# Optimization experiments

Hardware: AMD Instinct MI355X
Metric: run time of the kernel (lower is better)

## Reference

```python
import jax, jax.numpy as jnp
import numpy as np

B, N, D, K = 16, 1024, 512, 16  # batch graphs, nodes/graph, feat dim, knn k
NEG_SLOPE = 0.2


def setup_inputs() -> dict:
    key = jax.random.key(0)
    ks = jax.random.split(key, 16)
    s = 1.0 / np.sqrt(D)
    p = {}
    p["x"] = jax.random.normal(ks[0], (B, N, D), dtype=jnp.float32)
    for i, l in enumerate(["1", "2", "3"]):
        p["W" + l] = jax.random.normal(ks[1 + 4 * i], (D, D), dtype=jnp.float32) * s
        p["asrc" + l] = jax.random.normal(ks[2 + 4 * i], (D,), dtype=jnp.float32) * s
        p["adst" + l] = jax.random.normal(ks[3 + 4 * i], (D,), dtype=jnp.float32) * s
        p["b" + l] = jnp.zeros((D,), dtype=jnp.float32)
    p["Wc"] = jax.random.normal(ks[13], (D, 2), dtype=jnp.float32) * s
    p["bc"] = jnp.zeros((2,), dtype=jnp.float32)
    return p


def _knn_idx(pos):
    # pos: [N, D]. k nearest neighbors by euclidean distance, self excluded
    sq = jnp.sum(pos * pos, axis=1)
    d2 = sq[:, None] + sq[None, :] - 2.0 * (pos @ pos.T)  # [N, N]
    d2 = jnp.where(jnp.eye(N, dtype=bool), jnp.inf, d2)
    _, idx = jax.lax.top_k(-d2, K)  # [N, K] neighbor (source) indices per node
    return idx


def _normalize_scale(pos):
    # PyG NormalizeScale: center, then scale so max abs coord ~ 1
    pos = pos - pos.mean(axis=0, keepdims=True)
    return pos * (0.999999 / jnp.max(jnp.abs(pos)))


def _gat(h, nbr, W, asrc, adst, b):
    # GATConv, 1 head, self-loops already included in nbr [N, K+1]
    hp = h @ W                                   # [N, D]
    a_s = hp @ asrc                              # [N] att for sources
    a_d = hp @ adst                              # [N] att for targets
    e = jax.nn.leaky_relu(a_s[nbr] + a_d[:, None], NEG_SLOPE)  # [N, K+1]
    att = jax.nn.softmax(e, axis=-1)             # softmax over each node's in-edges
    msg = hp[nbr]                                # [N, K+1, D] gathered neighbor feats
    return jnp.einsum('nk,nkd->nd', att, msg) + b


def reference(x, W1, asrc1, adst1, b1, W2, asrc2, adst2, b2, W3, asrc3, adst3, b3, Wc, bc):
    self_idx = jnp.arange(N)[:, None]

    def per_graph(pos):
        nbr = jnp.concatenate([_knn_idx(pos), self_idx], axis=1)  # [N, K+1] w/ self-loop
        h = _normalize_scale(pos)
        h = jax.nn.relu(_gat(h, nbr, W1, asrc1, adst1, b1))
        h = jax.nn.relu(_gat(h, nbr, W2, asrc2, adst2, b2))
        h = _gat(h, nbr, W3, asrc3, adst3, b3)
        return h.max(axis=0)  # global max pool over nodes

    g = jax.vmap(per_graph)(x)  # [B, D]
    return g @ Wc + bc          # [B, 2]
```

## Files before the change

kernel.cpp:

```cpp
#include <hip/hip_runtime.h>
#include <hip/hip_bf16.h>
#include <math.h>

#define BATCH 16
#define NNODE 1024
#define DIM   512
#define KNN   16
#define KP1   17
#define NCAND 18
#define NEG   0.2f
#define BT    128
#define NCH   16

typedef __attribute__((ext_vector_type(8))) short bf16x8;
typedef __attribute__((ext_vector_type(4))) float f32x4;

#define GLOAD16(g, l) __builtin_amdgcn_global_load_lds( \
    (const __attribute__((address_space(1))) unsigned int*)(g), \
    (__attribute__((address_space(3))) unsigned int*)(l), 16, 0, 0)

__device__ __forceinline__ unsigned short f2bf(float f) {
    unsigned u = __float_as_uint(f);
    unsigned r = (u + 0x7FFFu + ((u >> 16) & 1u)) >> 16;
    return (unsigned short)r;
}
__device__ __forceinline__ float bf2f(unsigned short h) {
    return __uint_as_float(((unsigned)h) << 16);
}
__device__ __forceinline__ void split_store(float v, unsigned short* hi, unsigned short* lo, size_t idx) {
    unsigned short h = f2bf(v);
    hi[idx] = h;
    lo[idx] = f2bf(v - bf2f(h));
}

__global__ void init_misc(unsigned* __restrict__ maxabs, unsigned* __restrict__ genc) {
    int gid = blockIdx.x * 256 + threadIdx.x;
    if (gid < BATCH) maxabs[gid] = 0u;
    if (gid < BATCH * DIM) genc[gid] = 0u;
}

__global__ __launch_bounds__(256) void colmean_part(const float* __restrict__ x, float* __restrict__ part) {
    int b = blockIdx.x, dc = blockIdx.y, ch = blockIdx.z;
    int d = dc * 256 + threadIdx.x;
    const float* p = x + ((size_t)b * NNODE + ch * (NNODE / NCH)) * DIM + d;
    float s = 0.f;
    #pragma unroll 4
    for (int n = 0; n < NNODE / NCH; ++n) s += p[(size_t)n * DIM];
    part[((size_t)b * NCH + ch) * DIM + d] = s;
}
__global__ void colmean_fin(const float* __restrict__ part, float* __restrict__ mean) {
    int id = blockIdx.x * 256 + threadIdx.x;
    int b = id >> 9, d = id & (DIM - 1);
    float s = 0.f;
    #pragma unroll
    for (int ch = 0; ch < NCH; ++ch) s += part[((size_t)b * NCH + ch) * DIM + d];
    mean[id] = s * (1.0f / NNODE);
}

__global__ __launch_bounds__(256) void rowsq_xtobf(const float* __restrict__ x,
                                                   float* __restrict__ sq,
                                                   unsigned short* __restrict__ xh) {
    int row = blockIdx.x * 4 + (threadIdx.x >> 6);
    int l = threadIdx.x & 63;
    const float* p = x + (size_t)row * DIM + l * 8;
    float4 a = *(const float4*)p;
    float4 b = *(const float4*)(p + 4);
    float s = a.x * a.x + a.y * a.y + a.z * a.z + a.w * a.w
            + b.x * b.x + b.y * b.y + b.z * b.z + b.w * b.w;
    ushort4 ha, hb;
    ha.x = f2bf(a.x); ha.y = f2bf(a.y); ha.z = f2bf(a.z); ha.w = f2bf(a.w);
    hb.x = f2bf(b.x); hb.y = f2bf(b.y); hb.z = f2bf(b.z); hb.w = f2bf(b.w);
    unsigned short* q = xh + (size_t)row * DIM + l * 8;
    *(ushort4*)q = ha;
    *(ushort4*)(q + 4) = hb;
    #pragma unroll
    for (int off = 32; off > 0; off >>= 1) s += __shfl_down(s, off, 64);
    if (l == 0) sq[row] = s;
}

__global__ __launch_bounds__(256, 2) void dist_mfma(const unsigned short* __restrict__ xh,
                                                    const float* __restrict__ sq,
                                                    unsigned* __restrict__ keys) {
    __shared__ unsigned short AhL[128][32], BhL[128][32];
    int mt = blockIdx.y;
    int b = mt >> 3;
    int m0 = mt * BT;
    int n0 = blockIdx.x * BT;
    int bn0 = b * NNODE + n0;
    int t = threadIdx.x;
    int lane = t & 63, w = t >> 6;
    int wm = (w >> 1) * 64, wn = (w & 1) * 64;
    int fr = lane & 15, fk = (lane >> 4) * 8;
    f32x4 acc[4][4];
    #pragma unroll
    for (int i = 0; i < 4; ++i)
        #pragma unroll
        for (int j = 0; j < 4; ++j) acc[i][j] = (f32x4){0.f, 0.f, 0.f, 0.f};

    for (int k0 = 0; k0 < DIM; k0 += 32) {
        if (k0) __syncthreads();
        #pragma unroll
        for (int p = 0; p < 2; ++p) {
            int u = t + p * 256;
            int row = u >> 2, sl = u & 3;
            int gseg = (sl ^ ((row >> 1) & 3)) * 8;
            GLOAD16(xh + (size_t)(m0 + row) * DIM + k0 + gseg, &AhL[0][0] + u * 8);
            GLOAD16(xh + (size_t)(bn0 + row) * DIM + k0 + gseg, &BhL[0][0] + u * 8);
        }
        __syncthreads();
        bf16x8 ah[4], bh[4];
        #pragma unroll
        for (int i = 0; i < 4; ++i) {
            int ra = wm + i * 16 + fr;
            int sa = (((fk >> 3) ^ ((ra >> 1) & 3)) << 3);
            ah[i] = *(const bf16x8*)&AhL[ra][sa];
            int rb = wn + i * 16 + fr;
            int sb = (((fk >> 3) ^ ((rb >> 1) & 3)) << 3);
            bh[i] = *(const bf16x8*)&BhL[rb][sb];
        }
        #pragma unroll
        for (int i = 0; i < 4; ++i)
            #pragma unroll
            for (int j = 0; j < 4; ++j)
                acc[i][j] = __builtin_amdgcn_mfma_f32_16x16x32_bf16(ah[i], bh[j], acc[i][j], 0, 0, 0);
    }
    const float* sqb = sq + b * NNODE;
    int mloc0 = m0 - b * NNODE;
    #pragma unroll
    for (int i = 0; i < 4; ++i) {
        int mloc = mloc0 + wm + i * 16 + (lane >> 4) * 4;
        #pragma unroll
        for (int j = 0; j < 4; ++j) {
            int n = n0 + wn + j * 16 + fr;
            float sqn = sqb[n];
            #pragma unroll
            for (int r = 0; r < 4; ++r) {
                float val = sqb[mloc + r] + sqn - 2.f * acc[i][j][r];
                unsigned kv = (__float_as_uint(val) & 0xFFFFFC00u) | (unsigned)n;
                if (mloc + r == n) kv = 0xFFFFFFFFu;
                keys[((size_t)b * NNODE + mloc + r) * NNODE + n] = kv;
            }
        }
    }
}

__global__ __launch_bounds__(256) void knn_kernel(const unsigned* __restrict__ keys, int* __restrict__ cand) {
    int row = blockIdx.x * 4 + (threadIdx.x >> 6);
    int l = threadIdx.x & 63;
    const unsigned* src = keys + (size_t)row * NNODE;
    unsigned key[16];
    #pragma unroll
    for (int j = 0; j < 16; ++j) key[j] = src[l + (j << 6)];
    int* dst = cand + row * NCAND;
    unsigned T = 0;
    for (int it = 0; it < NCAND; ++it) {
        unsigned lmin = 0xFFFFFFFFu;
        #pragma unroll
        for (int j = 0; j < 16; ++j) {
            unsigned k = (key[j] > T) ? key[j] : 0xFFFFFFFFu;
            lmin = min(lmin, k);
        }
        #pragma unroll
        for (int off = 1; off < 64; off <<= 1) {
            unsigned o = (unsigned)__shfl_xor((int)lmin, off, 64);
            lmin = min(lmin, o);
        }
        T = lmin;
        if (l == 0) dst[it] = (int)(lmin & 1023u);
    }
}

__global__ __launch_bounds__(256) void rerank_kernel(const float* __restrict__ x,
                                                     const float* __restrict__ sq,
                                                     const int* __restrict__ cand,
                                                     int* __restrict__ nbr) {
    int bid = blockIdx.x;
    int b = bid & (BATCH - 1);
    int w = threadIdx.x >> 6, l = threadIdx.x & 63;
    int m = (bid >> 4) * 4 + w;
    int row = b * NNODE + m;
    const float* xb = x + (size_t)b * NNODE * DIM;
    const float* sqb = sq + b * NNODE;
    const float* xm = xb + (size_t)m * DIM;
    float4 m0v = *(const float4*)(xm + l * 8);
    float4 m1v = *(const float4*)(xm + l * 8 + 4);
    float sqm = sqb[m];

    int idx[NCAND];
    #pragma unroll
    for (int c = 0; c < NCAND; ++c) idx[c] = cand[row * NCAND + c];

    float s[NCAND];
    #pragma unroll
    for (int half = 0; half < 2; ++half) {
        float4 j0[9], j1[9];
        #pragma unroll
        for (int i = 0; i < 9; ++i) {
            const float* xj = xb + (size_t)idx[half * 9 + i] * DIM;
            j0[i] = *(const float4*)(xj + l * 8);
            j1[i] = *(const float4*)(xj + l * 8 + 4);
        }
        #pragma unroll
        for (int i = 0; i < 9; ++i)
            s[half * 9 + i] = m0v.x * j0[i].x + m0v.y * j0[i].y + m0v.z * j0[i].z + m0v.w * j0[i].w
                            + m1v.x * j1[i].x + m1v.y * j1[i].y + m1v.z * j1[i].z + m1v.w * j1[i].w;
    }
    #pragma unroll
    for (int off = 32; off > 0; off >>= 1)
        #pragma unroll
        for (int c = 0; c < NCAND; ++c) s[c] += __shfl_xor(s[c], off, 64);

    unsigned long long key[NCAND];
    #pragma unroll
    for (int c = 0; c < NCAND; ++c) {
        float dv = sqm + sqb[idx[c]] - 2.f * s[c];
        key[c] = ((unsigned long long)__float_as_uint(dv) << 32) | (unsigned)idx[c];
    }
    unsigned long long mykey = ~0ull;
    int myidx = 0;
    #pragma unroll
    for (int c = 0; c < NCAND; ++c) {
        if (l == c) { mykey = key[c]; myidx = idx[c]; }
    }
    int rank = 0;
    #pragma unroll
    for (int c = 0; c < NCAND; ++c) rank += (key[c] < mykey) ? 1 : 0;

    int* dst = nbr + row * KP1;
    if (l < NCAND && rank < KNN) dst[rank] = myidx;
    if (l == 0) dst[KNN] = m;
}

__global__ __launch_bounds__(256) void maxabs_kernel(const float* __restrict__ x,
                                                     const float* __restrict__ mean,
                                                     unsigned* __restrict__ maxabs) {
    int b = blockIdx.y;
    const float* p = x + ((size_t)b * NNODE + blockIdx.x * 64) * DIM;
    const float* mb = mean + b * DIM;
    float m = 0.f;
    for (int i = threadIdx.x; i < 64 * DIM; i += 256) {
        int d = i & (DIM - 1);
        m = fmaxf(m, fabsf(p[i] - mb[d]));
    }
    __shared__ float red[256];
    red[threadIdx.x] = m; __syncthreads();
    for (int s = 128; s > 0; s >>= 1) {
        if (threadIdx.x < s) red[threadIdx.x] = fmaxf(red[threadIdx.x], red[threadIdx.x + s]);
        __syncthreads();
    }
    if (threadIdx.x == 0) atomicMax(maxabs + b, __float_as_uint(red[0]));
}

__global__ void normalize_kernel(const float* __restrict__ x, const float* __restrict__ mean,
                                 const unsigned* __restrict__ maxabs,
                                 unsigned short* __restrict__ h_hi, unsigned short* __restrict__ h_lo) {
    int id = blockIdx.x * 256 + threadIdx.x;
    int b = id >> 19;
    int d = id & (DIM - 1);
    float scale = 0.999999f / __uint_as_float(maxabs[b]);
    float v = (x[id] - mean[b * DIM + d]) * scale;
    split_store(v, h_hi, h_lo, id);
}

__global__ void wsplit_kernel(const float* __restrict__ W1, const float* __restrict__ W2,
                              const float* __restrict__ W3,
                              unsigned short* __restrict__ Wh1, unsigned short* __restrict__ Wl1,
                              unsigned short* __restrict__ Wh2, unsigned short* __restrict__ Wl2,
                              unsigned short* __restrict__ Wh3, unsigned short* __restrict__ Wl3) {
    int z = blockIdx.z;
    const float* W = (z == 0) ? W1 : (z == 1) ? W2 : W3;
    unsigned short* Wh = (z == 0) ? Wh1 : (z == 1) ? Wh2 : Wh3;
    unsigned short* Wl = (z == 0) ? Wl1 : (z == 1) ? Wl2 : Wl3;
    __shared__ float tile[32][33];
    int bx = blockIdx.x * 32, by = blockIdx.y * 32;
    int tx = threadIdx.x & 31, ty = threadIdx.x >> 5;
    #pragma unroll
    for (int i = 0; i < 4; ++i)
        tile[ty + i * 8][tx] = W[(size_t)(by + ty + i * 8) * DIM + bx + tx];
    __syncthreads();
    #pragma unroll
    for (int i = 0; i < 4; ++i) {
        int n = bx + ty + i * 8;
        float v = tile[tx][ty + i * 8];
        split_store(v, Wh, Wl, (size_t)n * DIM + by + tx);
    }
}

__global__ __launch_bounds__(256, 2) void gemm_mfma(const unsigned short* __restrict__ Agh,
                                                    const unsigned short* __restrict__ Agl,
                                                    const unsigned short* __restrict__ Bgh,
                                                    const unsigned short* __restrict__ Bgl,
                                                    const float* __restrict__ asrc,
                                                    const float* __restrict__ adst,
                                                    float* __restrict__ C,
                                                    float* __restrict__ pas,
                                                    float* __restrict__ pad) {
    __shared__ unsigned short AhL[128][32], AlL[128][32], BhL[128][32], BlL[128][32];
    __shared__ float asl[128], adl[128];
    int m0 = blockIdx.y * BT, n0 = blockIdx.x * BT;
    int t = threadIdx.x;
    int lane = t & 63, w = t >> 6;
    int wm = (w >> 1) * 64, wn = (w & 1) * 64;
    int fr = lane & 15, fk = (lane >> 4) * 8;
    f32x4 acc[4][4];
    #pragma unroll
    for (int i = 0; i < 4; ++i)
        #pragma unroll
        for (int j = 0; j < 4; ++j) acc[i][j] = (f32x4){0.f, 0.f, 0.f, 0.f};

    for (int k0 = 0; k0 < DIM; k0 += 32) {
        if (k0) __syncthreads();
        #pragma unroll
        for (int p = 0; p < 2; ++p) {
            int u = t + p * 256;
            int row = u >> 2, sl = u & 3;
            int gseg = (sl ^ ((row >> 1) & 3)) * 8;
            size_t ga = (size_t)(m0 + row) * DIM + k0 + gseg;
            size_t gb = (size_t)(n0 + row) * DIM + k0 + gseg;
            GLOAD16(Agh + ga, &AhL[0][0] + u * 8);
            GLOAD16(Agl + ga, &AlL[0][0] + u * 8);
            GLOAD16(Bgh + gb, &BhL[0][0] + u * 8);
            GLOAD16(Bgl + gb, &BlL[0][0] + u * 8);
        }
        __syncthreads();
        bf16x8 ah[4], al[4], bh[4], bl[4];
        #pragma unroll
        for (int i = 0; i < 4; ++i) {
            int ra = wm + i * 16 + fr;
            int sa = (((fk >> 3) ^ ((ra >> 1) & 3)) << 3);
            ah[i] = *(const bf16x8*)&AhL[ra][sa];
            al[i] = *(const bf16x8*)&AlL[ra][sa];
            int rb = wn + i * 16 + fr;
            int sb = (((fk >> 3) ^ ((rb >> 1) & 3)) << 3);
            bh[i] = *(const bf16x8*)&BhL[rb][sb];
            bl[i] = *(const bf16x8*)&BlL[rb][sb];
        }
        #pragma unroll
        for (int i = 0; i < 4; ++i)
            #pragma unroll
            for (int j = 0; j < 4; ++j)
                acc[i][j] = __builtin_amdgcn_mfma_f32_16x16x32_bf16(ah[i], bh[j], acc[i][j], 0, 0, 0);
        #pragma unroll
        for (int i = 0; i < 4; ++i)
            #pragma unroll
            for (int j = 0; j < 4; ++j)
                acc[i][j] = __builtin_amdgcn_mfma_f32_16x16x32_bf16(ah[i], bl[j], acc[i][j], 0, 0, 0);
        #pragma unroll
        for (int i = 0; i < 4; ++i)
            #pragma unroll
            for (int j = 0; j < 4; ++j)
                acc[i][j] = __builtin_amdgcn_mfma_f32_16x16x32_bf16(al[i], bh[j], acc[i][j], 0, 0, 0);
    }
    #pragma unroll
    for (int i = 0; i < 4; ++i) {
        int mrow = m0 + wm + i * 16 + (lane >> 4) * 4;
        #pragma unroll
        for (int j = 0; j < 4; ++j) {
            int col = n0 + wn + j * 16 + fr;
            #pragma unroll
            for (int r = 0; r < 4; ++r)
                C[(size_t)(mrow + r) * DIM + col] = acc[i][j][r];
        }
    }
    float av[4], dv[4];
    #pragma unroll
    for (int j = 0; j < 4; ++j) {
        int col = n0 + wn + j * 16 + fr;
        av[j] = asrc[col];
        dv[j] = adst[col];
    }
    if (t < 128) { asl[t] = 0.f; adl[t] = 0.f; }
    __syncthreads();
    #pragma unroll
    for (int ph = 0; ph < 2; ++ph) {
        if ((wn == 0) == (ph == 0)) {
            #pragma unroll
            for (int i = 0; i < 4; ++i)
                #pragma unroll
                for (int r = 0; r < 4; ++r) {
                    float sa = acc[i][0][r] * av[0] + acc[i][1][r] * av[1]
                             + acc[i][2][r] * av[2] + acc[i][3][r] * av[3];
                    float sd = acc[i][0][r] * dv[0] + acc[i][1][r] * dv[1]
                             + acc[i][2][r] * dv[2] + acc[i][3][r] * dv[3];
                    #pragma unroll
                    for (int off = 1; off < 16; off <<= 1) {
                        sa += __shfl_xor(sa, off, 64);
                        sd += __shfl_xor(sd, off, 64);
                    }
                    if (fr == 0) {
                        int rloc = wm + i * 16 + (lane >> 4) * 4 + r;
                        if (ph == 0) { asl[rloc] = sa;  adl[rloc] = sd; }
                        else         { asl[rloc] += sa; adl[rloc] += sd; }
                    }
                }
        }
        __syncthreads();
    }
    if (t < 128) {
        pas[(size_t)(m0 + t) * 4 + blockIdx.x] = asl[t];
        pad[(size_t)(m0 + t) * 4 + blockIdx.x] = adl[t];
    }
}

__global__ void attvec_fin(const float* __restrict__ pas, const float* __restrict__ pad,
                           float* __restrict__ as_, float* __restrict__ ad_) {
    int id = blockIdx.x * 256 + threadIdx.x;
    float4 a = *(const float4*)(pas + (size_t)id * 4);
    float4 d = *(const float4*)(pad + (size_t)id * 4);
    as_[id] = ((a.x + a.y) + a.z) + a.w;
    ad_[id] = ((d.x + d.y) + d.z) + d.w;
}

template<int RELU, int SPLIT>
__global__ __launch_bounds__(256) void aggr_kernel(const float* __restrict__ hp, const int* __restrict__ nbr,
                                                   const float* __restrict__ as_, const float* __restrict__ ad_,
                                                   const float* __restrict__ bias,
                                                   float* __restrict__ outf,
                                                   unsigned short* __restrict__ oh,
                                                   unsigned short* __restrict__ ol) {
    __shared__ float attL[4][KP1];
    __shared__ int   jjL[4][KP1];
    int bid = blockIdx.x;
    int b = bid & (BATCH - 1);
    int w = threadIdx.x >> 6, l = threadIdx.x & 63;
    int n = (bid >> 4) * 4 + w;
    int id = b * NNODE + n;

    float e = -INFINITY;
    if (l < KP1) {
        int j = nbr[id * KP1 + l];
        jjL[w][l] = j;
        e = as_[b * NNODE + j] + ad_[id];
        e = (e >= 0.f) ? e : NEG * e;
    }
    float mx = e;
    #pragma unroll
    for (int off = 16; off > 0; off >>= 1) mx = fmaxf(mx, __shfl_xor(mx, off, 64));
    float ex = (l < KP1) ? expf(e - mx) : 0.f;
    float sm = ex;
    #pragma unroll
    for (int off = 16; off > 0; off >>= 1) sm += __shfl_xor(sm, off, 64);
    if (l < KP1) attL[w][l] = ex / sm;

    const float* base = hp + (size_t)b * NNODE * DIM;
    int d0 = l * 8;
    const float4* b4 = (const float4*)(bias + d0);
    float4 o0 = b4[0], o1 = b4[1];
    #pragma unroll
    for (int k = 0; k < KP1; ++k) {
        float a = attL[w][k];
        const float* vp = base + (size_t)jjL[w][k] * DIM + d0;
        float4 v0 = *(const float4*)vp;
        float4 v1 = *(const float4*)(vp + 4);
        o0.x += a * v0.x; o0.y += a * v0.y; o0.z += a * v0.z; o0.w += a * v0.w;
        o1.x += a * v1.x; o1.y += a * v1.y; o1.z += a * v1.z; o1.w += a * v1.w;
    }
    if (RELU) {
        o0.x = fmaxf(o0.x, 0.f); o0.y = fmaxf(o0.y, 0.f); o0.z = fmaxf(o0.z, 0.f); o0.w = fmaxf(o0.w, 0.f);
        o1.x = fmaxf(o1.x, 0.f); o1.y = fmaxf(o1.y, 0.f); o1.z = fmaxf(o1.z, 0.f); o1.w = fmaxf(o1.w, 0.f);
    }
    size_t idx = (size_t)id * DIM + d0;
    if (SPLIT) {
        float v[8] = {o0.x, o0.y, o0.z, o0.w, o1.x, o1.y, o1.z, o1.w};
        unsigned hi[4], lo[4];
        #pragma unroll
        for (int i = 0; i < 4; ++i) {
            unsigned short h0 = f2bf(v[2 * i]),     h1 = f2bf(v[2 * i + 1]);
            unsigned short l0 = f2bf(v[2 * i] - bf2f(h0));
            unsigned short l1 = f2bf(v[2 * i + 1] - bf2f(h1));
            hi[i] = (unsigned)h0 | ((unsigned)h1 << 16);
            lo[i] = (unsigned)l0 | ((unsigned)l1 << 16);
        }
        *(uint4*)(oh + idx) = *(uint4*)hi;
        *(uint4*)(ol + idx) = *(uint4*)lo;
    } else {
        *(float4*)(outf + idx) = o0;
        *(float4*)(outf + idx + 4) = o1;
    }
}

__global__ __launch_bounds__(256) void maxpool_atomic(const float* __restrict__ h, unsigned* __restrict__ genc) {
    int b = blockIdx.x, dc = blockIdx.y, ch = blockIdx.z;
    int d = dc * 256 + threadIdx.x;
    const float* p = h + ((size_t)b * NNODE + ch * (NNODE / NCH)) * DIM + d;
    float m = -INFINITY;
    #pragma unroll 4
    for (int n = 0; n < NNODE / NCH; ++n) m = fmaxf(m, p[(size_t)n * DIM]);
    unsigned u = __float_as_uint(m);
    unsigned enc = (u & 0x80000000u) ? ~u : (u | 0x80000000u);
    atomicMax(genc + b * DIM + d, enc);
}

__global__ void final_kernel(const unsigned* __restrict__ genc, const float* __restrict__ Wc,
                             const float* __restrict__ bc, float* __restrict__ out) {
    int b = blockIdx.x, t = threadIdx.x;
    float s0 = 0.f, s1 = 0.f;
    for (int d = t; d < DIM; d += 256) {
        unsigned e = genc[b * DIM + d];
        unsigned u = (e & 0x80000000u) ? (e ^ 0x80000000u) : ~e;
        float v = __uint_as_float(u);
        s0 += v * Wc[d * 2 + 0];
        s1 += v * Wc[d * 2 + 1];
    }
    __shared__ float r0[256], r1[256];
    r0[t] = s0; r1[t] = s1; __syncthreads();
    for (int s = 128; s > 0; s >>= 1) {
        if (t < s) { r0[t] += r0[t + s]; r1[t] += r1[t + s]; }
        __syncthreads();
    }
    if (t == 0) { out[b * 2] = r0[0] + bc[0]; out[b * 2 + 1] = r1[0] + bc[1]; }
}

extern "C" void kernel_launch(void* const* d_in, const int* in_sizes, int n_in,
                              void* d_out, int out_size, void* d_ws, size_t ws_size,
                              hipStream_t stream) {
    const float* x     = (const float*)d_in[0];
    const float* W1    = (const float*)d_in[1];
    const float* asrc1 = (const float*)d_in[2];
    const float* adst1 = (const float*)d_in[3];
    const float* b1    = (const float*)d_in[4];
    const float* W2    = (const float*)d_in[5];
    const float* asrc2 = (const float*)d_in[6];
    const float* adst2 = (const float*)d_in[7];
    const float* b2    = (const float*)d_in[8];
    const float* W3    = (const float*)d_in[9];
    const float* asrc3 = (const float*)d_in[10];
    const float* adst3 = (const float*)d_in[11];
    const float* b3    = (const float*)d_in[12];
    const float* Wc    = (const float*)d_in[13];
    const float* bc    = (const float*)d_in[14];
    float* out = (float*)d_out;

    char* ws = (char*)d_ws;
    unsigned*       keys  = (unsigned*)ws;
    float*          hp    = (float*)ws;
    unsigned short* hA_hi = (unsigned short*)(ws + (32ull << 20));
    unsigned short* hA_lo = (unsigned short*)(ws + (48ull << 20));
    unsigned short* xh    = (unsigned short*)(ws + (64ull << 20));
    unsigned short* hB_hi = (unsigned short*)(ws + (64ull << 20));
    unsigned short* hB_lo = (unsigned short*)(ws + (80ull << 20));
    float*          h3    = (float*)(ws + (64ull << 20));
    size_t off = 96ull << 20;
    unsigned short* Wt1h = (unsigned short*)(ws + off); off += (size_t)DIM * DIM * 2;
    unsigned short* Wt1l = (unsigned short*)(ws + off); off += (size_t)DIM * DIM * 2;
    unsigned short* Wt2h = (unsigned short*)(ws + off); off += (size_t)DIM * DIM * 2;
    unsigned short* Wt2l = (unsigned short*)(ws + off); off += (size_t)DIM * DIM * 2;
    unsigned short* Wt3h = (unsigned short*)(ws + off); off += (size_t)DIM * DIM * 2;
    unsigned short* Wt3l = (unsigned short*)(ws + off); off += (size_t)DIM * DIM * 2;
    int*      nbr    = (int*)(ws + off);      off += (size_t)BATCH * NNODE * KP1 * 4;
    int*      cand   = (int*)(ws + off);      off += (size_t)BATCH * NNODE * NCAND * 4;
    float*    sq     = (float*)(ws + off);    off += (size_t)BATCH * NNODE * 4;
    float*    mean   = (float*)(ws + off);    off += (size_t)BATCH * DIM * 4;
    unsigned* maxabs = (unsigned*)(ws + off); off += 256;
    float*    as_    = (float*)(ws + off);    off += (size_t)BATCH * NNODE * 4;
    float*    ad_    = (float*)(ws + off);    off += (size_t)BATCH * NNODE * 4;
    unsigned* genc   = (unsigned*)(ws + off); off += (size_t)BATCH * DIM * 4;
    float*    part   = (float*)(ws + off);    off += (size_t)BATCH * NCH * DIM * 4;
    float*    pas    = part;
    float*    pad    = part + (size_t)BATCH * NNODE * 4;
    (void)ws_size; (void)in_sizes; (void)n_in; (void)out_size;

    const dim3 cgrid(BATCH, DIM / 256, NCH);
    init_misc<<<32, 256, 0, stream>>>(maxabs, genc);
    colmean_part<<<cgrid, 256, 0, stream>>>(x, part);
    colmean_fin<<<BATCH * DIM / 256, 256, 0, stream>>>(part, mean);
    rowsq_xtobf<<<BATCH * NNODE / 4, 256, 0, stream>>>(x, sq, xh);
    dist_mfma<<<dim3(NNODE / BT, BATCH * NNODE / BT), 256, 0, stream>>>(xh, sq, keys);
    knn_kernel<<<BATCH * NNODE / 4, 256, 0, stream>>>(keys, cand);
    rerank_kernel<<<BATCH * NNODE / 4, 256, 0, stream>>>(x, sq, cand, nbr);
    wsplit_kernel<<<dim3(16, 16, 3), 256, 0, stream>>>(W1, W2, W3, Wt1h, Wt1l, Wt2h, Wt2l, Wt3h, Wt3l);
    maxabs_kernel<<<dim3(16, BATCH), 256, 0, stream>>>(x, mean, maxabs);
    normalize_kernel<<<BATCH * NNODE * DIM / 256, 256, 0, stream>>>(x, mean, maxabs, hA_hi, hA_lo);

    const dim3 ggrid(DIM / BT, BATCH * NNODE / BT);
    gemm_mfma<<<ggrid, 256, 0, stream>>>(hA_hi, hA_lo, Wt1h, Wt1l, asrc1, adst1, hp, pas, pad);
    attvec_fin<<<BATCH * NNODE / 256, 256, 0, stream>>>(pas, pad, as_, ad_);
    aggr_kernel<1, 1><<<BATCH * NNODE / 4, 256, 0, stream>>>(hp, nbr, as_, ad_, b1, nullptr, hB_hi, hB_lo);
    gemm_mfma<<<ggrid, 256, 0, stream>>>(hB_hi, hB_lo, Wt2h, Wt2l, asrc2, adst2, hp, pas, pad);
    attvec_fin<<<BATCH * NNODE / 256, 256, 0, stream>>>(pas, pad, as_, ad_);
    aggr_kernel<1, 1><<<BATCH * NNODE / 4, 256, 0, stream>>>(hp, nbr, as_, ad_, b2, nullptr, hA_hi, hA_lo);
    gemm_mfma<<<ggrid, 256, 0, stream>>>(hA_hi, hA_lo, Wt3h, Wt3l, asrc3, adst3, hp, pas, pad);
    attvec_fin<<<BATCH * NNODE / 256, 256, 0, stream>>>(pas, pad, as_, ad_);
    aggr_kernel<0, 0><<<BATCH * NNODE / 4, 256, 0, stream>>>(hp, nbr, as_, ad_, b3, h3, nullptr, nullptr);
    maxpool_atomic<<<cgrid, 256, 0, stream>>>(h3, genc);
    final_kernel<<<BATCH, 256, 0, stream>>>(genc, Wc, bc, out);
}
```

Before: 396.6 us.

## Double K-tile depth and remap blocks to XCDs in distance and GEMM kernels

Both MFMA kernels now stage 64-wide K slices instead of 32, with an 8-way XOR swizzle, which halves the number of barrier-separated iterations. The 2D grids become 1D grids whose block index is remapped so that consecutive blocks on the same XCD share M tiles, aiming for better L2 reuse of the A rows. LDS per block doubles, which may limit occupancy in the GEMM (64KB for four tiles), and the pas/pad column index is adjusted to use the remapped n-block.

```diff
diff --git a/kernel.cpp b/kernel.cpp
--- a/kernel.cpp
+++ b/kernel.cpp
@@ -81,11 +81,14 @@
 __global__ __launch_bounds__(256, 2) void dist_mfma(const unsigned short* __restrict__ xh,
                                                     const float* __restrict__ sq,
                                                     unsigned* __restrict__ keys) {
-    __shared__ unsigned short AhL[128][32], BhL[128][32];
-    int mt = blockIdx.y;
+    __shared__ unsigned short AhL[128][64], BhL[128][64];
+    int fh = blockIdx.x;
+    int xcd = fh & 7, ord = fh >> 3;
+    int mt = xcd * 16 + (ord >> 3);
+    int nb = ord & 7;
     int b = mt >> 3;
     int m0 = mt * BT;
-    int n0 = blockIdx.x * BT;
+    int n0 = nb * BT;
     int bn0 = b * NNODE + n0;
     int t = threadIdx.x;
     int lane = t & 63, w = t >> 6;
@@ -97,32 +100,34 @@
         #pragma unroll
         for (int j = 0; j < 4; ++j) acc[i][j] = (f32x4){0.f, 0.f, 0.f, 0.f};
 
-    for (int k0 = 0; k0 < DIM; k0 += 32) {
+    for (int k0 = 0; k0 < DIM; k0 += 64) {
         if (k0) __syncthreads();
         #pragma unroll
-        for (int p = 0; p < 2; ++p) {
+        for (int p = 0; p < 4; ++p) {
             int u = t + p * 256;
-            int row = u >> 2, sl = u & 3;
-            int gseg = (sl ^ ((row >> 1) & 3)) * 8;
+            int row = u >> 3, slot = u & 7;
+            int gseg = (slot ^ (row & 7)) * 8;
             GLOAD16(xh + (size_t)(m0 + row) * DIM + k0 + gseg, &AhL[0][0] + u * 8);
             GLOAD16(xh + (size_t)(bn0 + row) * DIM + k0 + gseg, &BhL[0][0] + u * 8);
         }
         __syncthreads();
-        bf16x8 ah[4], bh[4];
-        #pragma unroll
-        for (int i = 0; i < 4; ++i) {
-            int ra = wm + i * 16 + fr;
-            int sa = (((fk >> 3) ^ ((ra >> 1) & 3)) << 3);
-            ah[i] = *(const bf16x8*)&AhL[ra][sa];
-            int rb = wn + i * 16 + fr;
-            int sb = (((fk >> 3) ^ ((rb >> 1) & 3)) << 3);
-            bh[i] = *(const bf16x8*)&BhL[rb][sb];
-        }
-        #pragma unroll
-        for (int i = 0; i < 4; ++i)
-            #pragma unroll
-            for (int j = 0; j < 4; ++j)
-                acc[i][j] = __builtin_amdgcn_mfma_f32_16x16x32_bf16(ah[i], bh[j], acc[i][j], 0, 0, 0);
+        #pragma unroll
+        for (int s = 0; s < 2; ++s) {
+            bf16x8 ah[4], bh[4];
+            int ks = s * 4 + (fk >> 3);
+            #pragma unroll
+            for (int i = 0; i < 4; ++i) {
+                int ra = wm + i * 16 + fr;
+                ah[i] = *(const bf16x8*)&AhL[ra][(ks ^ (ra & 7)) * 8];
+                int rb = wn + i * 16 + fr;
+                bh[i] = *(const bf16x8*)&BhL[rb][(ks ^ (rb & 7)) * 8];
+            }
+            #pragma unroll
+            for (int i = 0; i < 4; ++i)
+                #pragma unroll
+                for (int j = 0; j < 4; ++j)
+                    acc[i][j] = __builtin_amdgcn_mfma_f32_16x16x32_bf16(ah[i], bh[j], acc[i][j], 0, 0, 0);
+        }
     }
     const float* sqb = sq + b * NNODE;
     int mloc0 = m0 - b * NNODE;
@@ -295,9 +300,13 @@
                                                     float* __restrict__ C,
                                                     float* __restrict__ pas,
                                                     float* __restrict__ pad) {
-    __shared__ unsigned short AhL[128][32], AlL[128][32], BhL[128][32], BlL[128][32];
+    __shared__ unsigned short AhL[128][64], AlL[128][64], BhL[128][64], BlL[128][64];
     __shared__ float asl[128], adl[128];
-    int m0 = blockIdx.y * BT, n0 = blockIdx.x * BT;
+    int fh = blockIdx.x;
+    int xcd = fh & 7, ord = fh >> 3;
+    int mt = xcd * 16 + (ord >> 2);
+    int nb = ord & 3;
+    int m0 = mt * BT, n0 = nb * BT;
     int t = threadIdx.x;
     int lane = t & 63, w = t >> 6;
     int wm = (w >> 1) * 64, wn = (w & 1) * 64;
@@ -308,13 +317,13 @@
         #pragma unroll
         for (int j = 0; j < 4; ++j) acc[i][j] = (f32x4){0.f, 0.f, 0.f, 0.f};
 
-    for (int k0 = 0; k0 < DIM; k0 += 32) {
+    for (int k0 = 0; k0 < DIM; k0 += 64) {
         if (k0) __syncthreads();
         #pragma unroll
-        for (int p = 0; p < 2; ++p) {
+        for (int p = 0; p < 4; ++p) {
             int u = t + p * 256;
-            int row = u >> 2, sl = u & 3;
-            int gseg = (sl ^ ((row >> 1) & 3)) * 8;
+            int row = u >> 3, slot = u & 7;
+            int gseg = (slot ^ (row & 7)) * 8;
             size_t ga = (size_t)(m0 + row) * DIM + k0 + gseg;
             size_t gb = (size_t)(n0 + row) * DIM + k0 + gseg;
             GLOAD16(Agh + ga, &AhL[0][0] + u * 8);
@@ -323,33 +332,37 @@
             GLOAD16(Bgl + gb, &BlL[0][0] + u * 8);
         }
         __syncthreads();
-        bf16x8 ah[4], al[4], bh[4], bl[4];
-        #pragma unroll
-        for (int i = 0; i < 4; ++i) {
-            int ra = wm + i * 16 + fr;
-            int sa = (((fk >> 3) ^ ((ra >> 1) & 3)) << 3);
-            ah[i] = *(const bf16x8*)&AhL[ra][sa];
-            al[i] = *(const bf16x8*)&AlL[ra][sa];
-            int rb = wn + i * 16 + fr;
-            int sb = (((fk >> 3) ^ ((rb >> 1) & 3)) << 3);
-            bh[i] = *(const bf16x8*)&BhL[rb][sb];
-            bl[i] = *(const bf16x8*)&BlL[rb][sb];
-        }
-        #pragma unroll
-        for (int i = 0; i < 4; ++i)
-            #pragma unroll
-            for (int j = 0; j < 4; ++j)
-                acc[i][j] = __builtin_amdgcn_mfma_f32_16x16x32_bf16(ah[i], bh[j], acc[i][j], 0, 0, 0);
-        #pragma unroll
-        for (int i = 0; i < 4; ++i)
-            #pragma unroll
-            for (int j = 0; j < 4; ++j)
-                acc[i][j] = __builtin_amdgcn_mfma_f32_16x16x32_bf16(ah[i], bl[j], acc[i][j], 0, 0, 0);
-        #pragma unroll
-        for (int i = 0; i < 4; ++i)
-            #pragma unroll
-            for (int j = 0; j < 4; ++j)
-                acc[i][j] = __builtin_amdgcn_mfma_f32_16x16x32_bf16(al[i], bh[j], acc[i][j], 0, 0, 0);
+        #pragma unroll
+        for (int s = 0; s < 2; ++s) {
+            bf16x8 ah[4], al[4], bh[4], bl[4];
+            int ks = s * 4 + (fk >> 3);
+            #pragma unroll
+            for (int i = 0; i < 4; ++i) {
+                int ra = wm + i * 16 + fr;
+                int sa = (ks ^ (ra & 7)) * 8;
+                ah[i] = *(const bf16x8*)&AhL[ra][sa];
+                al[i] = *(const bf16x8*)&AlL[ra][sa];
+                int rb = wn + i * 16 + fr;
+                int sb = (ks ^ (rb & 7)) * 8;
+                bh[i] = *(const bf16x8*)&BhL[rb][sb];
+                bl[i] = *(const bf16x8*)&BlL[rb][sb];
+            }
+            #pragma unroll
+            for (int i = 0; i < 4; ++i)
+                #pragma unroll
+                for (int j = 0; j < 4; ++j)
+                    acc[i][j] = __builtin_amdgcn_mfma_f32_16x16x32_bf16(ah[i], bh[j], acc[i][j], 0, 0, 0);
+            #pragma unroll
+            for (int i = 0; i < 4; ++i)
+                #pragma unroll
+                for (int j = 0; j < 4; ++j)
+                    acc[i][j] = __builtin_amdgcn_mfma_f32_16x16x32_bf16(ah[i], bl[j], acc[i][j], 0, 0, 0);
+            #pragma unroll
+            for (int i = 0; i < 4; ++i)
+                #pragma unroll
+                for (int j = 0; j < 4; ++j)
+                    acc[i][j] = __builtin_amdgcn_mfma_f32_16x16x32_bf16(al[i], bh[j], acc[i][j], 0, 0, 0);
+        }
     }
     #pragma unroll
     for (int i = 0; i < 4; ++i) {
@@ -397,8 +410,8 @@
         __syncthreads();
     }
     if (t < 128) {
-        pas[(size_t)(m0 + t) * 4 + blockIdx.x] = asl[t];
-        pad[(size_t)(m0 + t) * 4 + blockIdx.x] = adl[t];
+        pas[(size_t)(m0 + t) * 4 + nb] = asl[t];
+        pad[(size_t)(m0 + t) * 4 + nb] = adl[t];
     }
 }
 
@@ -565,14 +578,14 @@
     colmean_part<<<cgrid, 256, 0, stream>>>(x, part);
     colmean_fin<<<BATCH * DIM / 256, 256, 0, stream>>>(part, mean);
     rowsq_xtobf<<<BATCH * NNODE / 4, 256, 0, stream>>>(x, sq, xh);
-    dist_mfma<<<dim3(NNODE / BT, BATCH * NNODE / BT), 256, 0, stream>>>(xh, sq, keys);
+    dist_mfma<<<(NNODE / BT) * (BATCH * NNODE / BT), 256, 0, stream>>>(xh, sq, keys);
     knn_kernel<<<BATCH * NNODE / 4, 256, 0, stream>>>(keys, cand);
     rerank_kernel<<<BATCH * NNODE / 4, 256, 0, stream>>>(x, sq, cand, nbr);
     wsplit_kernel<<<dim3(16, 16, 3), 256, 0, stream>>>(W1, W2, W3, Wt1h, Wt1l, Wt2h, Wt2l, Wt3h, Wt3l);
     maxabs_kernel<<<dim3(16, BATCH), 256, 0, stream>>>(x, mean, maxabs);
     normalize_kernel<<<BATCH * NNODE * DIM / 256, 256, 0, stream>>>(x, mean, maxabs, hA_hi, hA_lo);
 
-    const dim3 ggrid(DIM / BT, BATCH * NNODE / BT);
+    const int ggrid = (DIM / BT) * (BATCH * NNODE / BT);
     gemm_mfma<<<ggrid, 256, 0, stream>>>(hA_hi, hA_lo, Wt1h, Wt1l, asrc1, adst1, hp, pas, pad);
     attvec_fin<<<BATCH * NNODE / 256, 256, 0, stream>>>(pas, pad, as_, ad_);
     aggr_kernel<1, 1><<<BATCH * NNODE / 4, 256, 0, stream>>>(hp, nbr, as_, ad_, b1, nullptr, hB_hi, hB_lo);
```

Result: faster. 367.6 us (median of 2 runs) (-7.3%).
